# Performance work log

Hardware: AMD Instinct MI355X
Metric: run time of the kernel (lower is better)

Reference implementation:

```python
import jax, jax.numpy as jnp
import numpy as np

MASK_PENALTY = 10000.0

def setup_inputs() -> dict:
    key = jax.random.key(0)
    kq, kk, kv = jax.random.split(key, 3)
    B, S, D = 8, 2048, 64
    return {
        "query": jax.random.normal(kq, (B, S, D), dtype=jnp.float32),
        "key": jax.random.normal(kk, (B, S, D), dtype=jnp.float32),
        "value": jax.random.normal(kv, (B, S, D), dtype=jnp.float32),
        "mask": jnp.ones((B, S), dtype=jnp.bool_),
    }

def reference(query, key, value, mask):
    # e: [B, Sq, Sk]
    d = query.shape[-1]
    e = jnp.einsum('bqd,bkd->bqk', query, key) / jnp.sqrt(jnp.float32(d))
    Sq, Sk = query.shape[1], key.shape[1]
    # history_only causal mask: key index > query index gets -10000
    causal = (jnp.arange(Sk)[None, :] > jnp.arange(Sq)[:, None]).astype(jnp.float32)
    e = e - MASK_PENALTY * causal[None, :, :]
    # padding mask: [B, Sk] -> [B, 1, Sk]
    e = e - MASK_PENALTY * (1.0 - mask.astype(jnp.float32))[:, None, :]
    attn = jax.nn.softmax(e, axis=-1)
    return jnp.einsum('bqk,bkd->bqd', attn, value)
```

## Files before the change

### kernel.cpp

```cpp
#include <hip/hip_runtime.h>


typedef _Float16 f16x8 __attribute__((ext_vector_type(8)));
typedef float    f32x4 __attribute__((ext_vector_type(4)));

#define MFMA16(A, B, C) __builtin_amdgcn_mfma_f32_16x16x32_f16(A, B, C, 0, 0, 0)

__device__ inline unsigned pack2h(float a, float b) {
    union { _Float16 h[2]; unsigned u; } t;
    t.h[0] = (_Float16)a; t.h[1] = (_Float16)b;
    return t.u;
}

constexpr int PSTR = 40;

__global__ __launch_bounds__(256, 4)
void prep_f16(const float* __restrict__ K, const float* __restrict__ V,
              _Float16* __restrict__ Kh, _Float16* __restrict__ Vt) {
    __shared__ _Float16 sT[64 * 72];
    const int b   = blockIdx.x >> 5;
    const int s0  = (blockIdx.x & 31) * 64;
    const int t   = threadIdx.x;
    const int row = t >> 2;
    const int grp = (t & 3) * 16;
    const size_t base = ((size_t)b * 2048 + s0 + row) * 64 + grp;
    {
        union { _Float16 h[16]; f16x8 v[2]; } o;
        const float* p = K + base;
#pragma unroll
        for (int i = 0; i < 16; i += 4) {
            float4 x = *(const float4*)(p + i);
            o.h[i] = (_Float16)x.x; o.h[i+1] = (_Float16)x.y;
            o.h[i+2] = (_Float16)x.z; o.h[i+3] = (_Float16)x.w;
        }
        *(f16x8*)(Kh + base) = o.v[0];
        *(f16x8*)(Kh + base + 8) = o.v[1];
    }
    {
        const float* p = V + base;
#pragma unroll
        for (int i = 0; i < 16; i += 4) {
            float4 x = *(const float4*)(p + i);
            sT[(grp + i    ) * 72 + row] = (_Float16)x.x;
            sT[(grp + i + 1) * 72 + row] = (_Float16)x.y;
            sT[(grp + i + 2) * 72 + row] = (_Float16)x.z;
            sT[(grp + i + 3) * 72 + row] = (_Float16)x.w;
        }
    }
    __syncthreads();
    {
        const size_t o = ((size_t)b * 64 + row) * 2048 + s0 + grp;
        *(f16x8*)(Vt + o)     = *(const f16x8*)&sT[row * 72 + grp];
        *(f16x8*)(Vt + o + 8) = *(const f16x8*)&sT[row * 72 + grp + 8];
    }
}

__global__ __launch_bounds__(512, 4)
void attn_f16_fast(const float* __restrict__ Q, const _Float16* __restrict__ Kh,
                   const _Float16* __restrict__ Vt, const int* __restrict__ M,
                   float* __restrict__ O) {
    constexpr int S = 2048, D = 64;
    constexpr float CSCALE = 0.18033688011112042f;

    __shared__ __align__(16) _Float16 sP[8][16 * PSTR];
    __shared__ float sO[8][16 * 64];
    __shared__ float sL[8][16];

    const int tid  = threadIdx.x;
    const int w    = tid >> 6;
    const int lane = tid & 63;
    const int l15  = lane & 15;
    const int quad = lane >> 4;

    for (int phase = 0; phase < 2; ++phase) {
        const int batch = (int)blockIdx.y ^ phase;
        const int tile  = phase ? 127 - (int)blockIdx.x : (int)blockIdx.x;
        const int n_kt  = tile / 2 + 1;
        const int qg0   = tile * 16;
        const size_t bq = (size_t)batch * S;
        const _Float16* Kb = Kh + bq * D;
        const _Float16* Vb = Vt + (size_t)batch * D * S;

        f16x8 qf[2];
        {
            const float* qp = Q + (bq + qg0 + l15) * D + quad * 8;
#pragma unroll
            for (int dc = 0; dc < 2; ++dc) {
                float4 x0 = *(const float4*)(qp + dc * 32);
                float4 x1 = *(const float4*)(qp + dc * 32 + 4);
                union { unsigned u[4]; f16x8 v; } t;
                t.u[0] = pack2h(x0.x, x0.y); t.u[1] = pack2h(x0.z, x0.w);
                t.u[2] = pack2h(x1.x, x1.y); t.u[3] = pack2h(x1.z, x1.w);
                qf[dc] = t.v;
            }
        }

        f32x4 acc[4]; float lacc[4];
#pragma unroll
        for (int c = 0; c < 4; ++c) { acc[c][0] = acc[c][1] = acc[c][2] = acc[c][3] = 0.f; }
#pragma unroll
        for (int r = 0; r < 4; ++r) lacc[r] = 0.f;

        f16x8 kn[2][2], vn[4]; int m0n = 0, m1n = 0;
        if (w < n_kt) {
            const int kb = w * 32;
#pragma unroll
            for (int kg = 0; kg < 2; ++kg)
#pragma unroll
                for (int dc = 0; dc < 2; ++dc)
                    kn[kg][dc] = *(const f16x8*)(Kb + (size_t)(kb + kg * 16 + l15) * D + dc * 32 + quad * 8);
#pragma unroll
            for (int c = 0; c < 4; ++c)
                vn[c] = *(const f16x8*)(Vb + (size_t)(c * 16 + l15) * S + kb + quad * 8);
            m0n = M[bq + kb + l15];
            m1n = M[bq + kb + 16 + l15];
        }

        for (int t = w; t < n_kt; t += 8) {
            const int kb = t * 32;
            f16x8 kf00 = kn[0][0], kf01 = kn[0][1], kf10 = kn[1][0], kf11 = kn[1][1];
            f16x8 vf0 = vn[0], vf1 = vn[1], vf2 = vn[2], vf3 = vn[3];
            const int m0c = m0n, m1c = m1n;
            if (t + 8 < n_kt) {
                const int kb2 = kb + 256;
#pragma unroll
                for (int kg = 0; kg < 2; ++kg)
#pragma unroll
                    for (int dc = 0; dc < 2; ++dc)
                        kn[kg][dc] = *(const f16x8*)(Kb + (size_t)(kb2 + kg * 16 + l15) * D + dc * 32 + quad * 8);
#pragma unroll
                for (int c = 0; c < 4; ++c)
                    vn[c] = *(const f16x8*)(Vb + (size_t)(c * 16 + l15) * S + kb2 + quad * 8);
                m0n = M[bq + kb2 + l15];
                m1n = M[bq + kb2 + 16 + l15];
            }

            f32x4 sc[2];
            {
                f32x4 z; z[0] = z[1] = z[2] = z[3] = 0.f;
                f32x4 y = MFMA16(qf[0], kf00, z);
                sc[0] = MFMA16(qf[1], kf01, y);
                f32x4 y2 = MFMA16(qf[0], kf10, z);
                sc[1] = MFMA16(qf[1], kf11, y2);
            }

            float p[2][4];
#pragma unroll
            for (int kg = 0; kg < 2; ++kg) {
                const int key = kb + kg * 16 + l15;
                const int mv  = kg ? m1c : m0c;
#pragma unroll
                for (int r = 0; r < 4; ++r) {
                    const int qrow = qg0 + quad * 4 + r;
                    float e  = __builtin_amdgcn_exp2f(sc[kg][r] * CSCALE);
                    bool  ok = (key <= qrow) && (mv != 0);
                    float pv = ok ? e : 0.f;
                    p[kg][r] = pv;
                    lacc[r] += pv;
                }
            }

            _Float16* sPw = sP[w];
#pragma unroll
            for (int kg = 0; kg < 2; ++kg)
#pragma unroll
                for (int r = 0; r < 4; ++r)
                    sPw[(quad * 4 + r) * PSTR + kg * 16 + l15] = (_Float16)p[kg][r];
            f16x8 pf = *(const f16x8*)(&sPw[l15 * PSTR + quad * 8]);

            acc[0] = MFMA16(pf, vf0, acc[0]);
            acc[1] = MFMA16(pf, vf1, acc[1]);
            acc[2] = MFMA16(pf, vf2, acc[2]);
            acc[3] = MFMA16(pf, vf3, acc[3]);
        }

#pragma unroll
        for (int r = 0; r < 4; ++r) {
            float s = lacc[r];
            s += __shfl_xor(s, 1, 64);
            s += __shfl_xor(s, 2, 64);
            s += __shfl_xor(s, 4, 64);
            s += __shfl_xor(s, 8, 64);
            lacc[r] = s;
        }

#pragma unroll
        for (int c = 0; c < 4; ++c)
#pragma unroll
            for (int r = 0; r < 4; ++r)
                sO[w][(quad * 4 + r) * 64 + c * 16 + l15] = acc[c][r];
        if (l15 == 0) {
#pragma unroll
            for (int r = 0; r < 4; ++r) sL[w][quad * 4 + r] = lacc[r];
        }
        __syncthreads();
        {
            const int row = tid >> 5;
            const int col = (tid & 31) * 2;
            float a = 0.f, b = 0.f, l = 0.f;
#pragma unroll
            for (int w2 = 0; w2 < 8; ++w2) {
                a += sO[w2][row * 64 + col];
                b += sO[w2][row * 64 + col + 1];
                l += sL[w2][row];
            }
            const float inv = 1.f / fmaxf(l, 1e-37f);
            float2 o; o.x = a * inv; o.y = b * inv;
            *(float2*)(&O[(bq + qg0 + row) * D + col]) = o;
        }
        __syncthreads();
    }
}

__global__ __launch_bounds__(512, 4)
void attn_f16_slow(const float* __restrict__ Q, const float* __restrict__ K,
                   const float* __restrict__ V, const int* __restrict__ M,
                   float* __restrict__ O) {
    constexpr int S = 2048, D = 64;
    constexpr float CSCALE = 0.18033688011112042f;
    __shared__ __align__(16) _Float16 sP[8][16 * PSTR];
    __shared__ float sO[8][16 * 64];
    __shared__ float sL[8][16];
    const int tid = threadIdx.x, w = tid >> 6, lane = tid & 63;
    const int l15 = lane & 15, quad = lane >> 4;
    for (int phase = 0; phase < 2; ++phase) {
        const int batch = (int)blockIdx.y ^ phase;
        const int tile  = phase ? 127 - (int)blockIdx.x : (int)blockIdx.x;
        const int n_kt  = tile / 2 + 1;
        const int qg0   = tile * 16;
        const size_t bq = (size_t)batch * S;
        f16x8 qf[2];
        {
            const float* qp = Q + (bq + qg0 + l15) * D + quad * 8;
#pragma unroll
            for (int dc = 0; dc < 2; ++dc) {
                float4 x0 = *(const float4*)(qp + dc * 32);
                float4 x1 = *(const float4*)(qp + dc * 32 + 4);
                union { unsigned u[4]; f16x8 v; } t;
                t.u[0] = pack2h(x0.x, x0.y); t.u[1] = pack2h(x0.z, x0.w);
                t.u[2] = pack2h(x1.x, x1.y); t.u[3] = pack2h(x1.z, x1.w);
                qf[dc] = t.v;
            }
        }
        f32x4 acc[4]; float lacc[4];
#pragma unroll
        for (int c = 0; c < 4; ++c) { acc[c][0] = acc[c][1] = acc[c][2] = acc[c][3] = 0.f; }
#pragma unroll
        for (int r = 0; r < 4; ++r) lacc[r] = 0.f;
        for (int t = w; t < n_kt; t += 8) {
            const int kb = t * 32;
            f16x8 kf[2][2];
            {
                const float* kp = K + (bq + kb + l15) * D + quad * 8;
#pragma unroll
                for (int kg = 0; kg < 2; ++kg)
#pragma unroll
                    for (int dc = 0; dc < 2; ++dc) {
                        float4 x0 = *(const float4*)(kp + kg * 16 * D + dc * 32);
                        float4 x1 = *(const float4*)(kp + kg * 16 * D + dc * 32 + 4);
                        union { unsigned u[4]; f16x8 v; } tt;
                        tt.u[0] = pack2h(x0.x, x0.y); tt.u[1] = pack2h(x0.z, x0.w);
                        tt.u[2] = pack2h(x1.x, x1.y); tt.u[3] = pack2h(x1.z, x1.w);
                        kf[kg][dc] = tt.v;
                    }
            }
            float vr[4][8];
            {
                const float* vp = V + (bq + kb + quad * 8) * D + l15;
#pragma unroll
                for (int c = 0; c < 4; ++c)
#pragma unroll
                    for (int j = 0; j < 8; ++j)
                        vr[c][j] = vp[j * D + c * 16];
            }
            const int m0 = M[bq + kb + l15];
            const int m1 = M[bq + kb + 16 + l15];
            f32x4 sc[2];
#pragma unroll
            for (int kg = 0; kg < 2; ++kg) {
                f32x4 z; z[0] = z[1] = z[2] = z[3] = 0.f;
                z = MFMA16(qf[0], kf[kg][0], z);
                sc[kg] = MFMA16(qf[1], kf[kg][1], z);
            }
            float p[2][4];
#pragma unroll
            for (int kg = 0; kg < 2; ++kg) {
                const int key = kb + kg * 16 + l15;
                const int mv  = kg ? m1 : m0;
#pragma unroll
                for (int r = 0; r < 4; ++r) {
                    const int qrow = qg0 + quad * 4 + r;
                    float e  = __builtin_amdgcn_exp2f(sc[kg][r] * CSCALE);
                    bool  ok = (key <= qrow) && (mv != 0);
                    float pv = ok ? e : 0.f;
                    p[kg][r] = pv;
                    lacc[r] += pv;
                }
            }
            _Float16* sPw = sP[w];
#pragma unroll
            for (int kg = 0; kg < 2; ++kg)
#pragma unroll
                for (int r = 0; r < 4; ++r)
                    sPw[(quad * 4 + r) * PSTR + kg * 16 + l15] = (_Float16)p[kg][r];
            f16x8 pf = *(const f16x8*)(&sPw[l15 * PSTR + quad * 8]);
#pragma unroll
            for (int c = 0; c < 4; ++c) {
                union { unsigned u[4]; f16x8 v; } tt;
                tt.u[0] = pack2h(vr[c][0], vr[c][1]);
                tt.u[1] = pack2h(vr[c][2], vr[c][3]);
                tt.u[2] = pack2h(vr[c][4], vr[c][5]);
                tt.u[3] = pack2h(vr[c][6], vr[c][7]);
                acc[c] = MFMA16(pf, tt.v, acc[c]);
            }
        }
#pragma unroll
        for (int r = 0; r < 4; ++r) {
            float s = lacc[r];
            s += __shfl_xor(s, 1, 64);
            s += __shfl_xor(s, 2, 64);
            s += __shfl_xor(s, 4, 64);
            s += __shfl_xor(s, 8, 64);
            lacc[r] = s;
        }
#pragma unroll
        for (int c = 0; c < 4; ++c)
#pragma unroll
            for (int r = 0; r < 4; ++r)
                sO[w][(quad * 4 + r) * 64 + c * 16 + l15] = acc[c][r];
        if (l15 == 0) {
#pragma unroll
            for (int r = 0; r < 4; ++r) sL[w][quad * 4 + r] = lacc[r];
        }
        __syncthreads();
        {
            const int row = tid >> 5;
            const int col = (tid & 31) * 2;
            float a = 0.f, b = 0.f, l = 0.f;
#pragma unroll
            for (int w2 = 0; w2 < 8; ++w2) {
                a += sO[w2][row * 64 + col];
                b += sO[w2][row * 64 + col + 1];
                l += sL[w2][row];
            }
            const float inv = 1.f / fmaxf(l, 1e-37f);
            float2 o; o.x = a * inv; o.y = b * inv;
            *(float2*)(&O[(bq + qg0 + row) * D + col]) = o;
        }
        __syncthreads();
    }
}

extern "C" void kernel_launch(void* const* d_in, const int* in_sizes, int n_in,
                              void* d_out, int out_size, void* d_ws, size_t ws_size,
                              hipStream_t stream) {
    const float* Q = (const float*)d_in[0];
    const float* K = (const float*)d_in[1];
    const float* V = (const float*)d_in[2];
    const int*   M = (const int*)d_in[3];
    float*       O = (float*)d_out;
    const size_t n_kv = (size_t)8 * 2048 * 64;
    const size_t need = n_kv * 2 * sizeof(_Float16);
    if (ws_size >= need) {
        _Float16* Kh = (_Float16*)d_ws;
        _Float16* Vt = Kh + n_kv;
        hipLaunchKernelGGL(prep_f16, dim3(256), dim3(256), 0, stream, K, V, Kh, Vt);
        hipLaunchKernelGGL(attn_f16_fast, dim3(64, 8), dim3(512), 0, stream, Q, Kh, Vt, M, O);
    } else {
        hipLaunchKernelGGL(attn_f16_slow, dim3(64, 8), dim3(512), 0, stream, Q, K, V, M, O);
    }
}
```

Baseline: 106.8 us.

## Compute transposed scores to keep P in registers and drop LDS round-trip

The attention kernel now computes S^T (K as the A operand, Q as B), so each lane holds a contiguous run of four keys for one query row. Those probabilities feed 16x16x16 MFMAs against V directly, which removes the per-tile shared-memory write/read of P. The phase-paired balancing loop is replaced by one block per query tile (grid 128x8, heaviest tiles first), the register prefetch of the next K/V tile is dropped, and launch bounds are raised to 5 blocks. This trades the old explicit load balancing and prefetch for more blocks, higher occupancy and twice as many smaller PV MFMAs.

```diff
diff --git a/kernel.cpp b/kernel.cpp
--- a/kernel.cpp
+++ b/kernel.cpp
@@ -2,17 +2,17 @@
 
 
 typedef _Float16 f16x8 __attribute__((ext_vector_type(8)));
+typedef _Float16 f16x4 __attribute__((ext_vector_type(4)));
 typedef float    f32x4 __attribute__((ext_vector_type(4)));
 
-#define MFMA16(A, B, C) __builtin_amdgcn_mfma_f32_16x16x32_f16(A, B, C, 0, 0, 0)
+#define MFMA_K32(A, B, C) __builtin_amdgcn_mfma_f32_16x16x32_f16(A, B, C, 0, 0, 0)
+#define MFMA_K16(A, B, C) __builtin_amdgcn_mfma_f32_16x16x16f16(A, B, C, 0, 0, 0)
 
 __device__ inline unsigned pack2h(float a, float b) {
     union { _Float16 h[2]; unsigned u; } t;
     t.h[0] = (_Float16)a; t.h[1] = (_Float16)b;
     return t.u;
 }
-
-constexpr int PSTR = 40;
 
 __global__ __launch_bounds__(256, 4)
 void prep_f16(const float* __restrict__ K, const float* __restrict__ V,
@@ -55,14 +55,13 @@
     }
 }
 
-__global__ __launch_bounds__(512, 4)
-void attn_f16_fast(const float* __restrict__ Q, const _Float16* __restrict__ Kh,
-                   const _Float16* __restrict__ Vt, const int* __restrict__ M,
-                   float* __restrict__ O) {
+__global__ __launch_bounds__(512, 5)
+void attn_f16_v3(const float* __restrict__ Q, const _Float16* __restrict__ Kh,
+                 const _Float16* __restrict__ Vt, const int* __restrict__ M,
+                 float* __restrict__ O) {
     constexpr int S = 2048, D = 64;
     constexpr float CSCALE = 0.18033688011112042f;
 
-    __shared__ __align__(16) _Float16 sP[8][16 * PSTR];
     __shared__ float sO[8][16 * 64];
     __shared__ float sL[8][16];
 
@@ -72,146 +71,111 @@
     const int l15  = lane & 15;
     const int quad = lane >> 4;
 
-    for (int phase = 0; phase < 2; ++phase) {
-        const int batch = (int)blockIdx.y ^ phase;
-        const int tile  = phase ? 127 - (int)blockIdx.x : (int)blockIdx.x;
-        const int n_kt  = tile / 2 + 1;
-        const int qg0   = tile * 16;
-        const size_t bq = (size_t)batch * S;
-        const _Float16* Kb = Kh + bq * D;
-        const _Float16* Vb = Vt + (size_t)batch * D * S;
-
-        f16x8 qf[2];
-        {
-            const float* qp = Q + (bq + qg0 + l15) * D + quad * 8;
-#pragma unroll
-            for (int dc = 0; dc < 2; ++dc) {
-                float4 x0 = *(const float4*)(qp + dc * 32);
-                float4 x1 = *(const float4*)(qp + dc * 32 + 4);
-                union { unsigned u[4]; f16x8 v; } t;
-                t.u[0] = pack2h(x0.x, x0.y); t.u[1] = pack2h(x0.z, x0.w);
-                t.u[2] = pack2h(x1.x, x1.y); t.u[3] = pack2h(x1.z, x1.w);
-                qf[dc] = t.v;
-            }
-        }
-
-        f32x4 acc[4]; float lacc[4];
-#pragma unroll
-        for (int c = 0; c < 4; ++c) { acc[c][0] = acc[c][1] = acc[c][2] = acc[c][3] = 0.f; }
-#pragma unroll
-        for (int r = 0; r < 4; ++r) lacc[r] = 0.f;
-
-        f16x8 kn[2][2], vn[4]; int m0n = 0, m1n = 0;
-        if (w < n_kt) {
-            const int kb = w * 32;
-#pragma unroll
-            for (int kg = 0; kg < 2; ++kg)
-#pragma unroll
-                for (int dc = 0; dc < 2; ++dc)
-                    kn[kg][dc] = *(const f16x8*)(Kb + (size_t)(kb + kg * 16 + l15) * D + dc * 32 + quad * 8);
+    const int tile  = 127 - (int)blockIdx.x;
+    const int batch = (int)blockIdx.y;
+    const int n_kt  = tile / 2 + 1;
+    const int qg0   = tile * 16;
+    const size_t bq = (size_t)batch * S;
+    const _Float16* Kb = Kh + bq * D;
+    const _Float16* Vb = Vt + (size_t)batch * D * S;
+
+    f16x8 qf[2];
+    {
+        const float* qp = Q + (bq + qg0 + l15) * D + quad * 8;
+#pragma unroll
+        for (int dc = 0; dc < 2; ++dc) {
+            float4 x0 = *(const float4*)(qp + dc * 32);
+            float4 x1 = *(const float4*)(qp + dc * 32 + 4);
+            union { unsigned u[4]; f16x8 v; } t;
+            t.u[0] = pack2h(x0.x, x0.y); t.u[1] = pack2h(x0.z, x0.w);
+            t.u[2] = pack2h(x1.x, x1.y); t.u[3] = pack2h(x1.z, x1.w);
+            qf[dc] = t.v;
+        }
+    }
+
+    f32x4 acc[4];
+    float lacc = 0.f;
+#pragma unroll
+    for (int c = 0; c < 4; ++c) { acc[c][0] = acc[c][1] = acc[c][2] = acc[c][3] = 0.f; }
+
+    for (int t = w; t < n_kt; t += 8) {
+        const int kb = t * 32;
+
+        f16x8 kf[2][2];
+#pragma unroll
+        for (int kg = 0; kg < 2; ++kg)
+#pragma unroll
+            for (int dc = 0; dc < 2; ++dc)
+                kf[kg][dc] = *(const f16x8*)(Kb + (size_t)(kb + kg * 16 + l15) * D + dc * 32 + quad * 8);
+
+        f16x4 vf[2][4];
+#pragma unroll
+        for (int kg = 0; kg < 2; ++kg)
 #pragma unroll
             for (int c = 0; c < 4; ++c)
-                vn[c] = *(const f16x8*)(Vb + (size_t)(c * 16 + l15) * S + kb + quad * 8);
-            m0n = M[bq + kb + l15];
-            m1n = M[bq + kb + 16 + l15];
-        }
-
-        for (int t = w; t < n_kt; t += 8) {
-            const int kb = t * 32;
-            f16x8 kf00 = kn[0][0], kf01 = kn[0][1], kf10 = kn[1][0], kf11 = kn[1][1];
-            f16x8 vf0 = vn[0], vf1 = vn[1], vf2 = vn[2], vf3 = vn[3];
-            const int m0c = m0n, m1c = m1n;
-            if (t + 8 < n_kt) {
-                const int kb2 = kb + 256;
-#pragma unroll
-                for (int kg = 0; kg < 2; ++kg)
-#pragma unroll
-                    for (int dc = 0; dc < 2; ++dc)
-                        kn[kg][dc] = *(const f16x8*)(Kb + (size_t)(kb2 + kg * 16 + l15) * D + dc * 32 + quad * 8);
-#pragma unroll
-                for (int c = 0; c < 4; ++c)
-                    vn[c] = *(const f16x8*)(Vb + (size_t)(c * 16 + l15) * S + kb2 + quad * 8);
-                m0n = M[bq + kb2 + l15];
-                m1n = M[bq + kb2 + 16 + l15];
-            }
-
-            f32x4 sc[2];
-            {
-                f32x4 z; z[0] = z[1] = z[2] = z[3] = 0.f;
-                f32x4 y = MFMA16(qf[0], kf00, z);
-                sc[0] = MFMA16(qf[1], kf01, y);
-                f32x4 y2 = MFMA16(qf[0], kf10, z);
-                sc[1] = MFMA16(qf[1], kf11, y2);
-            }
-
-            float p[2][4];
-#pragma unroll
-            for (int kg = 0; kg < 2; ++kg) {
-                const int key = kb + kg * 16 + l15;
-                const int mv  = kg ? m1c : m0c;
-#pragma unroll
-                for (int r = 0; r < 4; ++r) {
-                    const int qrow = qg0 + quad * 4 + r;
-                    float e  = __builtin_amdgcn_exp2f(sc[kg][r] * CSCALE);
-                    bool  ok = (key <= qrow) && (mv != 0);
-                    float pv = ok ? e : 0.f;
-                    p[kg][r] = pv;
-                    lacc[r] += pv;
-                }
-            }
-
-            _Float16* sPw = sP[w];
-#pragma unroll
-            for (int kg = 0; kg < 2; ++kg)
-#pragma unroll
-                for (int r = 0; r < 4; ++r)
-                    sPw[(quad * 4 + r) * PSTR + kg * 16 + l15] = (_Float16)p[kg][r];
-            f16x8 pf = *(const f16x8*)(&sPw[l15 * PSTR + quad * 8]);
-
-            acc[0] = MFMA16(pf, vf0, acc[0]);
-            acc[1] = MFMA16(pf, vf1, acc[1]);
-            acc[2] = MFMA16(pf, vf2, acc[2]);
-            acc[3] = MFMA16(pf, vf3, acc[3]);
-        }
-
-#pragma unroll
-        for (int r = 0; r < 4; ++r) {
-            float s = lacc[r];
-            s += __shfl_xor(s, 1, 64);
-            s += __shfl_xor(s, 2, 64);
-            s += __shfl_xor(s, 4, 64);
-            s += __shfl_xor(s, 8, 64);
-            lacc[r] = s;
-        }
-
-#pragma unroll
-        for (int c = 0; c < 4; ++c)
-#pragma unroll
-            for (int r = 0; r < 4; ++r)
-                sO[w][(quad * 4 + r) * 64 + c * 16 + l15] = acc[c][r];
-        if (l15 == 0) {
-#pragma unroll
-            for (int r = 0; r < 4; ++r) sL[w][quad * 4 + r] = lacc[r];
-        }
-        __syncthreads();
-        {
-            const int row = tid >> 5;
-            const int col = (tid & 31) * 2;
-            float a = 0.f, b = 0.f, l = 0.f;
-#pragma unroll
-            for (int w2 = 0; w2 < 8; ++w2) {
-                a += sO[w2][row * 64 + col];
-                b += sO[w2][row * 64 + col + 1];
-                l += sL[w2][row];
-            }
-            const float inv = 1.f / fmaxf(l, 1e-37f);
-            float2 o; o.x = a * inv; o.y = b * inv;
-            *(float2*)(&O[(bq + qg0 + row) * D + col]) = o;
-        }
-        __syncthreads();
-    }
-}
-
+                vf[kg][c] = *(const f16x4*)(Vb + (size_t)(c * 16 + l15) * S + kb + kg * 16 + quad * 4);
+
+        union { int a[4]; int4 v; } mq[2];
+        mq[0].v = *(const int4*)(M + bq + kb + quad * 4);
+        mq[1].v = *(const int4*)(M + bq + kb + 16 + quad * 4);
+
+        f32x4 scT[2];
+#pragma unroll
+        for (int kg = 0; kg < 2; ++kg) {
+            f32x4 z; z[0] = z[1] = z[2] = z[3] = 0.f;
+            z = MFMA_K32(kf[kg][0], qf[0], z);
+            scT[kg] = MFMA_K32(kf[kg][1], qf[1], z);
+        }
+
+        f16x4 pf[2];
+#pragma unroll
+        for (int kg = 0; kg < 2; ++kg) {
+            union { _Float16 h[4]; f16x4 v; } pp;
+#pragma unroll
+            for (int r = 0; r < 4; ++r) {
+                const int key = kb + kg * 16 + quad * 4 + r;
+                float e  = __builtin_amdgcn_exp2f(scT[kg][r] * CSCALE);
+                bool  ok = (key <= qg0 + l15) && (mq[kg].a[r] != 0);
+                float pv = ok ? e : 0.f;
+                lacc += pv;
+                pp.h[r] = (_Float16)pv;
+            }
+            pf[kg] = pp.v;
+        }
+
+#pragma unroll
+        for (int c = 0; c < 4; ++c) acc[c] = MFMA_K16(pf[0], vf[0][c], acc[c]);
+#pragma unroll
+        for (int c = 0; c < 4; ++c) acc[c] = MFMA_K16(pf[1], vf[1][c], acc[c]);
+    }
+
+    lacc += __shfl_xor(lacc, 16, 64);
+    lacc += __shfl_xor(lacc, 32, 64);
+
+#pragma unroll
+    for (int c = 0; c < 4; ++c)
+#pragma unroll
+        for (int r = 0; r < 4; ++r)
+            sO[w][(quad * 4 + r) * 64 + c * 16 + l15] = acc[c][r];
+    if (lane < 16) sL[w][l15] = lacc;
+    __syncthreads();
+    {
+        const int row = tid >> 5;
+        const int col = (tid & 31) * 2;
+        float a = 0.f, b = 0.f, l = 0.f;
+#pragma unroll
+        for (int w2 = 0; w2 < 8; ++w2) {
+            a += sO[w2][row * 64 + col];
+            b += sO[w2][row * 64 + col + 1];
+            l += sL[w2][row];
+        }
+        const float inv = 1.f / fmaxf(l, 1e-37f);
+        float2 o; o.x = a * inv; o.y = b * inv;
+        *(float2*)(&O[(bq + qg0 + row) * D + col]) = o;
+    }
+}
+
+constexpr int PSTR = 40;
 __global__ __launch_bounds__(512, 4)
 void attn_f16_slow(const float* __restrict__ Q, const float* __restrict__ K,
                    const float* __restrict__ V, const int* __restrict__ M,
@@ -279,8 +243,8 @@
 #pragma unroll
             for (int kg = 0; kg < 2; ++kg) {
                 f32x4 z; z[0] = z[1] = z[2] = z[3] = 0.f;
-                z = MFMA16(qf[0], kf[kg][0], z);
-                sc[kg] = MFMA16(qf[1], kf[kg][1], z);
+                z = MFMA_K32(qf[0], kf[kg][0], z);
+                sc[kg] = MFMA_K32(qf[1], kf[kg][1], z);
             }
             float p[2][4];
 #pragma unroll
@@ -311,7 +275,7 @@
                 tt.u[1] = pack2h(vr[c][2], vr[c][3]);
                 tt.u[2] = pack2h(vr[c][4], vr[c][5]);
                 tt.u[3] = pack2h(vr[c][6], vr[c][7]);
-                acc[c] = MFMA16(pf, tt.v, acc[c]);
+                acc[c] = MFMA_K32(pf, tt.v, acc[c]);
             }
         }
 #pragma unroll
@@ -365,7 +329,7 @@
         _Float16* Kh = (_Float16*)d_ws;
         _Float16* Vt = Kh + n_kv;
         hipLaunchKernelGGL(prep_f16, dim3(256), dim3(256), 0, stream, K, V, Kh, Vt);
-        hipLaunchKernelGGL(attn_f16_fast, dim3(64, 8), dim3(512), 0, stream, Q, Kh, Vt, M, O);
+        hipLaunchKernelGGL(attn_f16_v3, dim3(128, 8), dim3(512), 0, stream, Q, Kh, Vt, M, O);
     } else {
         hipLaunchKernelGGL(attn_f16_slow, dim3(64, 8), dim3(512), 0, stream, Q, K, V, M, O);
     }
```

After: 144.7 us. +35.5%, slower.
